# Performance work log

Measured on AMD Instinct MI355X. Metric: run time of the kernel, lower is better.

The kernel has to match this reference:

```python
import jax, jax.numpy as jnp
import numpy as np
from jax import lax

B, S, E, DF, H, L, V, T = 32, 512, 512, 2048, 8, 2, 30000, 12
START, STOP = 10, 11
NEG = -10000.0


def setup_inputs() -> dict:
    key = jax.random.key(0)
    ks = jax.random.split(key, 12)
    g = lambda i, shape, sc=0.02: jax.random.normal(ks[i], shape, jnp.float32) * sc
    trans = jax.random.normal(ks[9], (T, T), jnp.float32)
    trans = trans.at[START, :].set(NEG).at[:, STOP].set(NEG)
    return {
        "sentence": jax.random.randint(ks[0], (B, S), 0, V),
        "seq_len": jax.random.randint(ks[1], (B,), 1, S + 1),
        "tags": jax.random.randint(ks[2], (B, S), 0, 10),
        "emb": g(3, (V, E), 1.0),
        "attn_in_w": g(4, (L, 3 * E, E)), "attn_in_b": jnp.zeros((L, 3 * E)),
        "attn_out_w": g(5, (L, E, E)), "attn_out_b": jnp.zeros((L, E)),
        "ln1_g": jnp.ones((L, E)), "ln1_b": jnp.zeros((L, E)),
        "ln2_g": jnp.ones((L, E)), "ln2_b": jnp.zeros((L, E)),
        "ff1_w": g(6, (L, DF, E)), "ff1_b": jnp.zeros((L, DF)),
        "ff2_w": g(7, (L, E, DF)), "ff2_b": jnp.zeros((L, E)),
        "tag_w": g(8, (T, E)), "tag_b": jnp.zeros((T,)),
        "transitions": trans,
    }


def _ln(x, g, b):
    m = x.mean(-1, keepdims=True)
    v = ((x - m) ** 2).mean(-1, keepdims=True)
    return (x - m) / jnp.sqrt(v + 1e-5) * g + b


def _mha(x, w_in, b_in, w_out, b_out):
    b_, s_, e_ = x.shape
    d = e_ // H
    qkv = x @ w_in.T + b_in
    q, k, v = jnp.split(qkv, 3, axis=-1)
    split = lambda t: t.reshape(b_, s_, H, d).transpose(0, 2, 1, 3)
    q, k, v = split(q), split(k), split(v)
    att = jax.nn.softmax(jnp.einsum('bhqd,bhkd->bhqk', q, k) / np.sqrt(d).astype(np.float32), axis=-1)
    o = jnp.einsum('bhqk,bhkd->bhqd', att, v).transpose(0, 2, 1, 3).reshape(b_, s_, e_)
    return o @ w_out.T + b_out


def _forward_impl(sentence, seq_len, tags, emb, attn_in_w, attn_in_b, attn_out_w,
                  attn_out_b, ln1_g, ln1_b, ln2_g, ln2_b, ff1_w, ff1_b, ff2_w,
                  ff2_b, tag_w, tag_b, transitions):
    # Transformer encoder features (dropout in eval mode -> identity)
    x = emb[sentence]  # (B,S,E)
    for l in range(L):
        x = _ln(x + _mha(x, attn_in_w[l], attn_in_b[l], attn_out_w[l], attn_out_b[l]), ln1_g[l], ln1_b[l])
        h = jax.nn.relu(x @ ff1_w[l].T + ff1_b[l]) @ ff2_w[l].T + ff2_b[l]
        x = _ln(x + h, ln2_g[l], ln2_b[l])
    feats = x @ tag_w.T + tag_b  # (B,S,T)

    # CRF forward algorithm (log-semiring scan, masked by seq_len)
    alpha0 = jnp.full((B, T), NEG, feats.dtype).at[:, START].set(0.0)

    def step(alpha, xs):
        emit_t, t = xs  # emit_t: (B,T)
        new = emit_t + jax.nn.logsumexp(alpha[:, None, :] + transitions[None, :, :], axis=-1)
        return jnp.where((t < seq_len)[:, None], new, alpha), None

    alpha, _ = lax.scan(step, alpha0, (feats.transpose(1, 0, 2), jnp.arange(S)))
    fwd_score = jax.nn.logsumexp(alpha + transitions[STOP][None, :], axis=-1)  # (B,)

    # gold score (vectorized _score_sentence)
    tags_ext = jnp.concatenate([jnp.full((B, 1), START, tags.dtype), tags], axis=1)  # (B,S+1)
    mask = jnp.arange(S)[None, :] < seq_len[:, None]  # (B,S)
    trans_sc = jnp.where(mask, transitions[tags_ext[:, 1:], tags_ext[:, :-1]], 0.0).sum(-1)
    emit_sc = jnp.where(mask, jnp.take_along_axis(feats, tags[:, :, None], axis=2)[..., 0], 0.0).sum(-1)
    last_tag = jnp.take_along_axis(tags_ext, seq_len[:, None], axis=1)[:, 0]
    gold = trans_sc + emit_sc + transitions[STOP, last_tag]

    return jnp.mean(fwd_score - gold)


def reference(sentence, seq_len, tags, emb, attn_in_w, attn_in_b, attn_out_w,
              attn_out_b, ln1_g, ln1_b, ln2_g, ln2_b, ff1_w, ff1_b, ff2_w,
              ff2_b, tag_w, tag_b, transitions):
    return _forward_impl(sentence, seq_len, tags, emb, attn_in_w, attn_in_b,
                         attn_out_w, attn_out_b, ln1_g, ln1_b, ln2_g, ln2_b,
                         ff1_w, ff1_b, ff2_w, ff2_b, tag_w, tag_b, transitions)
```

## Files before the change

### kernel.cpp

```cpp
#include <hip/hip_runtime.h>
#include <hip/hip_bf16.h>

#define BB 32
#define SSZ 512
#define EE 512
#define DFF 2048
#define HH 8
#define LL 2
#define TT 12
#define START_TAG 10
#define STOP_TAG 11
#define CB 8
#define CM (CB * SSZ)
#define NCHUNK (BB / CB)
#define NBH (CB * HH)
#define NBH_ALL (BB * HH)
#define NCHK 8

typedef __hip_bfloat16 bf16;
typedef __attribute__((ext_vector_type(8))) short short8;
typedef __attribute__((ext_vector_type(4))) float f32x4;

__device__ __forceinline__ float b2f(bf16 x) { return __bfloat162float(x); }
__device__ __forceinline__ float ldw(const void* p, size_t i, bool isbf) {
  return isbf ? __bfloat162float(((const bf16*)p)[i]) : ((const float*)p)[i];
}

__device__ __forceinline__ void gl_lds16(const bf16* g, bf16* l) {
  __builtin_amdgcn_global_load_lds(
      (const __attribute__((address_space(1))) void*)g,
      (__attribute__((address_space(3))) void*)l, 16, 0, 0);
}

__device__ __forceinline__ void stg128(const bf16* __restrict__ G, int ldk,
                                       int row0, int col0, bf16* lds0,
                                       int w, int l) {
#pragma unroll
  for (int q = 0; q < 2; ++q) {
    int lr = q * 64 + w * 8 + (l >> 3);
    int gs = (l & 7) ^ (lr & 7);
    gl_lds16(G + (size_t)(row0 + lr) * ldk + col0 + gs * 8,
             lds0 + (q * 64 + w * 8) * 64);
  }
}

__device__ __forceinline__ short8 ldfrag(const bf16* T, int row, int gr) {
  return *(const short8*)&T[row * 64 + ((gr ^ (row & 7)) << 3)];
}

__global__ void k_detect(const void* trans, int* dflag) {
  if (threadIdx.x == 0) {
    const unsigned short* u = (const unsigned short*)trans;
    dflag[0] = (u[START_TAG * TT] == 0xC61C && u[START_TAG * TT + 1] == 0xC61C) ? 1 : 0;
  }
}

__global__ void k_cvt(const void* src, bf16* dst, long n, const int* dflag) {
  bool isbf = dflag[0] != 0;
  for (long i = (long)blockIdx.x * 256 + threadIdx.x; i < n; i += (long)gridDim.x * 256)
    dst[i] = __float2bfloat16(ldw(src, i, isbf));
}

__global__ void k_embed(const int* sent, const void* emb, bf16* xb, const int* dflag) {
  bool isbf = dflag[0] != 0;
  int tok = blockIdx.x;
  int v = sent[tok];
  bf16* xo = xb + (size_t)tok * EE;
  for (int i = threadIdx.x; i < EE; i += 256)
    xo[i] = __float2bfloat16(ldw(emb, (size_t)v * EE + i, isbf));
}

template <int BN>
__global__ __launch_bounds__(512, 2) void k_mgemm256(
    const bf16* __restrict__ A, const bf16* __restrict__ W,
    const void* __restrict__ bias, size_t boff, bf16* __restrict__ Cb,
    bf16* __restrict__ vtout, int M, int N, int K, int relu,
    const int* __restrict__ dflag) {
  constexpr int WN = BN / 64;
  constexpr int WM = 8 / WN;
  constexpr int RPW = 256 / WM;
  constexpr int MFR = RPW / 16;
  constexpr int QW = MFR / 4;
  constexpr int BH = BN / 128;
  constexpr int BUFSZ = 16384 + BN * 64;
  extern __shared__ __align__(16) bf16 Sh[];
  const bool isbf = dflag[0] != 0;
  const int tid = threadIdx.x;
  const int l = tid & 63;
  const int w = tid >> 6;
  const int wm = w / WN, wn = w % WN;
  const int lrow = l & 15, lk = l >> 4;
  const int m0 = blockIdx.x * 256, n0 = blockIdx.y * BN;

  f32x4 acc[MFR][4];
#pragma unroll
  for (int i = 0; i < MFR; ++i)
#pragma unroll
    for (int j = 0; j < 4; ++j) acc[i][j] = (f32x4){0.f, 0.f, 0.f, 0.f};

  const int NIT = K >> 7;

#pragma unroll
  for (int p = 0; p < 2; ++p) {
    bf16* Ab = Sh + p * BUFSZ;
    bf16* Bb = Ab + 16384;
    stg128(A, K, m0, p * 64, Ab, w, l);
    stg128(A, K, m0 + 128, p * 64, Ab + 8192, w, l);
#pragma unroll
    for (int h = 0; h < BH; ++h)
      stg128(W, K, n0 + h * 128, p * 64, Bb + h * 8192, w, l);
  }
  if (BN == 256) asm volatile("s_waitcnt vmcnt(8)" ::: "memory");
  else asm volatile("s_waitcnt vmcnt(6)" ::: "memory");
  __builtin_amdgcn_sched_barrier(0);
  __builtin_amdgcn_s_barrier();

#define LDAQ(q)                                                               \
  do {                                                                        \
    _Pragma("unroll") for (int mi = 0; mi < QW; ++mi)                         \
        _Pragma("unroll") for (int kb = 0; kb < 2; ++kb)                      \
            aq[q][mi][kb] = ldfrag(                                           \
                Ab, wm * RPW + ((q)*QW + mi) * 16 + lrow, kb * 4 + lk);       \
  } while (0)

#define MMQ(q)                                                                \
  do {                                                                        \
    __builtin_amdgcn_s_setprio(1);                                            \
    _Pragma("unroll") for (int mi = 0; mi < QW; ++mi)                         \
        _Pragma("unroll") for (int kb = 0; kb < 2; ++kb)                      \
            _Pragma("unroll") for (int nf = 0; nf < 4; ++nf)                  \
                acc[(q)*QW + mi][nf] =                                        \
                    __builtin_amdgcn_mfma_f32_16x16x32_bf16(                  \
                        aq[q][mi][kb], bfr[kb][nf], acc[(q)*QW + mi][nf],     \
                        0, 0, 0);                                             \
    __builtin_amdgcn_s_setprio(0);                                            \
  } while (0)

#pragma unroll 1
  for (int i = 0; i < NIT; ++i) {
    const bool more = (i + 1 < NIT);
#pragma unroll
    for (int hh = 0; hh < 2; ++hh) {
      bf16* Ab = Sh + hh * BUFSZ;
      bf16* Bb = Ab + 16384;
      const int kc2 = (2 * i + 2 + hh) << 6;
      short8 bfr[2][4];
      short8 aq[4][QW][2];
#pragma unroll
      for (int kb = 0; kb < 2; ++kb)
#pragma unroll
        for (int nf = 0; nf < 4; ++nf)
          bfr[kb][nf] = ldfrag(Bb, wn * 64 + nf * 16 + lrow, kb * 4 + lk);
      LDAQ(0);
      MMQ(0);
      __builtin_amdgcn_s_barrier();
      LDAQ(1);
      LDAQ(2);
      MMQ(1);
      __builtin_amdgcn_s_barrier();
      LDAQ(3);
      if (more) {
#pragma unroll
        for (int h = 0; h < BH; ++h)
          stg128(W, K, n0 + h * 128, kc2, Bb + h * 8192, w, l);
      }
      MMQ(2);
      asm volatile("s_waitcnt lgkmcnt(0)" ::: "memory");
      __builtin_amdgcn_sched_barrier(0);
      __builtin_amdgcn_s_barrier();
      if (more) {
        stg128(A, K, m0, kc2, Ab, w, l);
        stg128(A, K, m0 + 128, kc2, Ab + 8192, w, l);
      }
      MMQ(3);
      if (more) {
        if (BN == 256) asm volatile("s_waitcnt vmcnt(8)" ::: "memory");
        else asm volatile("s_waitcnt vmcnt(6)" ::: "memory");
      } else {
        asm volatile("s_waitcnt vmcnt(0)" ::: "memory");
      }
      __builtin_amdgcn_sched_barrier(0);
      __builtin_amdgcn_s_barrier();
    }
  }
#undef LDAQ
#undef MMQ

  const bool vpath = (BN == 256) && (vtout != nullptr) && (n0 >= 1024);
  if (!vpath) {
#pragma unroll
    for (int nf = 0; nf < 4; ++nf) {
      const int c = wn * 64 + nf * 16 + lrow;
      const float bia = ldw(bias, boff + n0 + c, isbf);
#pragma unroll
      for (int mf = 0; mf < MFR; ++mf)
#pragma unroll
        for (int r = 0; r < 4; ++r) {
          const int row = wm * RPW + mf * 16 + lk * 4 + r;
          float v = acc[mf][nf][r] + bia;
          if (relu) v = fmaxf(v, 0.f);
          Sh[row * BN + (c ^ (((row >> 2) & 7) << 4))] = __float2bfloat16(v);
        }
    }
    __syncthreads();
    constexpr int GPR = BN / 8;
    constexpr int RPP = 512 / GPR;
#pragma unroll
    for (int p = 0; p < 256 / RPP; ++p) {
      const int row = p * RPP + tid / GPR;
      const int g = tid % GPR;
      *(uint4*)(Cb + (size_t)(m0 + row) * N + n0 + g * 8) =
          *(const uint4*)&Sh[row * BN + ((g * 8) ^ (((row >> 2) & 7) << 4))];
    }
  } else {
    const int pos0 = m0 & 511;
    const int blb = (m0 >> 9) * 8;
#pragma unroll
    for (int nf = 0; nf < 4; ++nf) {
      const int c = wn * 64 + nf * 16 + lrow;
      const float bia = ldw(bias, boff + n0 + c, isbf);
#pragma unroll
      for (int mf = 0; mf < MFR; ++mf)
#pragma unroll
        for (int r = 0; r < 4; ++r) {
          const int row = wm * RPW + mf * 16 + lk * 4 + r;
          Sh[c * 256 + (row ^ (((c >> 2) & 7) << 4))] =
              __float2bfloat16(acc[mf][nf][r] + bia);
        }
    }
    __syncthreads();
#pragma unroll
    for (int p = 0; p < 16; ++p) {
      const int cc = p * 16 + (tid >> 5);
      const int g = tid & 31;
      const int vc = n0 - 1024 + cc;
      *(uint4*)(vtout + ((size_t)(blb + (vc >> 6)) * 64 + (vc & 63)) * 512 +
                pos0 + g * 8) =
          *(const uint4*)&Sh[cc * 256 + ((g * 8) ^ (((cc >> 2) & 7) << 4))];
    }
  }
}

#define LDK 68
#define LDP 72
__global__ __launch_bounds__(256) void k_flash(const bf16* __restrict__ qkv,
                                               const bf16* __restrict__ vt,
                                               bf16* __restrict__ ctx) {
  const int bh = blockIdx.x;
  const int bl = bh >> 3, h = bh & 7;
  const int m0 = blockIdx.y * 128;
  const int tid = threadIdx.x;
  const int lane = tid & 63;
  const int w = tid >> 6;
  const int lrow = lane & 15, lk = lane >> 4;

  __shared__ bf16 Ks[64 * LDK];
  __shared__ bf16 Vs[64 * LDK];
  __shared__ bf16 Ps[4][32 * LDP];

  short8 qf[2][2];
  {
    const bf16* Qb = qkv + (size_t)(bl * SSZ + m0 + w * 32) * 1536 + h * 64;
#pragma unroll
    for (int mf = 0; mf < 2; ++mf)
#pragma unroll
      for (int kb = 0; kb < 2; ++kb)
        qf[mf][kb] = *(const short8*)(Qb + (size_t)(mf * 16 + lrow) * 1536 + kb * 32 + lk * 8);
  }

  f32x4 acc_o[2][4];
  float lsum[2][4];
#pragma unroll
  for (int mf = 0; mf < 2; ++mf) {
#pragma unroll
    for (int nf = 0; nf < 4; ++nf) acc_o[mf][nf] = (f32x4){0.f, 0.f, 0.f, 0.f};
#pragma unroll
    for (int r = 0; r < 4; ++r) lsum[mf][r] = 0.f;
  }

  for (int kt = 0; kt < 8; ++kt) {
#pragma unroll
    for (int i = 0; i < 2; ++i) {
      int cc = tid + i * 256;
      int row = cc >> 3, seg = cc & 7;
      *(uint4*)&Ks[row * LDK + seg * 8] = *(const uint4*)(
          qkv + (size_t)(bl * SSZ + kt * 64 + row) * 1536 + 512 + h * 64 + seg * 8);
      *(uint4*)&Vs[row * LDK + seg * 8] = *(const uint4*)(
          vt + ((size_t)bh * 64 + row) * SSZ + kt * 64 + seg * 8);
    }
    __syncthreads();
    f32x4 s[2][4];
#pragma unroll
    for (int mf = 0; mf < 2; ++mf)
#pragma unroll
      for (int nf = 0; nf < 4; ++nf) s[mf][nf] = (f32x4){0.f, 0.f, 0.f, 0.f};
#pragma unroll
    for (int kb = 0; kb < 2; ++kb) {
      short8 bk[4];
#pragma unroll
      for (int nf = 0; nf < 4; ++nf)
        bk[nf] = *(const short8*)&Ks[(nf * 16 + lrow) * LDK + kb * 32 + lk * 8];
#pragma unroll
      for (int mf = 0; mf < 2; ++mf)
#pragma unroll
        for (int nf = 0; nf < 4; ++nf)
          s[mf][nf] = __builtin_amdgcn_mfma_f32_16x16x32_bf16(qf[mf][kb], bk[nf],
                                                              s[mf][nf], 0, 0, 0);
    }
#pragma unroll
    for (int mf = 0; mf < 2; ++mf)
#pragma unroll
      for (int r = 0; r < 4; ++r) {
        float p0 = __expf(0.125f * s[mf][0][r]);
        float p1 = __expf(0.125f * s[mf][1][r]);
        float p2 = __expf(0.125f * s[mf][2][r]);
        float p3 = __expf(0.125f * s[mf][3][r]);
        s[mf][0][r] = p0; s[mf][1][r] = p1; s[mf][2][r] = p2; s[mf][3][r] = p3;
        lsum[mf][r] += (p0 + p1) + (p2 + p3);
      }
#pragma unroll
    for (int mf = 0; mf < 2; ++mf)
#pragma unroll
      for (int nf = 0; nf < 4; ++nf)
#pragma unroll
        for (int r = 0; r < 4; ++r)
          Ps[w][(mf * 16 + lk * 4 + r) * LDP + nf * 16 + lrow] =
              __float2bfloat16(s[mf][nf][r]);
#pragma unroll
    for (int kb = 0; kb < 2; ++kb) {
      short8 ap[2], bv[4];
#pragma unroll
      for (int mf = 0; mf < 2; ++mf)
        ap[mf] = *(const short8*)&Ps[w][(mf * 16 + lrow) * LDP + kb * 32 + lk * 8];
#pragma unroll
      for (int nf = 0; nf < 4; ++nf)
        bv[nf] = *(const short8*)&Vs[(nf * 16 + lrow) * LDK + kb * 32 + lk * 8];
#pragma unroll
      for (int mf = 0; mf < 2; ++mf)
#pragma unroll
        for (int nf = 0; nf < 4; ++nf)
          acc_o[mf][nf] = __builtin_amdgcn_mfma_f32_16x16x32_bf16(ap[mf], bv[nf],
                                                                  acc_o[mf][nf], 0, 0, 0);
    }
    __syncthreads();
  }
#pragma unroll
  for (int mf = 0; mf < 2; ++mf) {
#pragma unroll
    for (int r = 0; r < 4; ++r) {
      float ls = lsum[mf][r];
      ls += __shfl_xor(ls, 1, 64);
      ls += __shfl_xor(ls, 2, 64);
      ls += __shfl_xor(ls, 4, 64);
      ls += __shfl_xor(ls, 8, 64);
      float inv = 1.f / ls;
      int q = m0 + w * 32 + mf * 16 + lk * 4 + r;
#pragma unroll
      for (int nf = 0; nf < 4; ++nf)
        ctx[((size_t)(bl * SSZ + q)) * EE + h * 64 + nf * 16 + lrow] =
            __float2bfloat16(acc_o[mf][nf][r] * inv);
    }
  }
}

__global__ void k_ln_res(bf16* xb, const bf16* hb, const void* g,
                         const void* be, size_t goff, const int* dflag) {
  bool isbf = dflag[0] != 0;
  int tok = blockIdx.x, tid = threadIdx.x;
  size_t base = (size_t)tok * EE;
  float v0 = b2f(xb[base + tid]) + b2f(hb[base + tid]);
  float v1 = b2f(xb[base + tid + 256]) + b2f(hb[base + tid + 256]);
  float s = v0 + v1, ss = v0 * v0 + v1 * v1;
#pragma unroll
  for (int off = 32; off > 0; off >>= 1) {
    s += __shfl_down(s, off, 64);
    ss += __shfl_down(ss, off, 64);
  }
  __shared__ float ps[4], pss[4];
  __shared__ float mean_s, rstd_s;
  int w = tid >> 6;
  if ((tid & 63) == 0) { ps[w] = s; pss[w] = ss; }
  __syncthreads();
  if (tid == 0) {
    float S_ = ps[0] + ps[1] + ps[2] + ps[3];
    float SS_ = pss[0] + pss[1] + pss[2] + pss[3];
    float mu = S_ / (float)EE;
    float var = SS_ / (float)EE - mu * mu;
    mean_s = mu;
    rstd_s = rsqrtf(var + 1e-5f);
  }
  __syncthreads();
  float mu = mean_s, rs = rstd_s;
  float r0 = (v0 - mu) * rs * ldw(g, goff + tid, isbf) + ldw(be, goff + tid, isbf);
  float r1 = (v1 - mu) * rs * ldw(g, goff + tid + 256, isbf) + ldw(be, goff + tid + 256, isbf);
  xb[base + tid] = __float2bfloat16(r0);
  xb[base + tid + 256] = __float2bfloat16(r1);
}

__global__ void k_feats(const bf16* xb, const bf16* tgw, const void* tgb,
                        float* feats, const int* dflag) {
  bool isbf = dflag[0] != 0;
  int m = blockIdx.x * 4 + (threadIdx.x >> 6);
  int lane = threadIdx.x & 63;
  uint4 raw = *(const uint4*)(xb + (size_t)m * EE + lane * 8);
  const bf16* rb = (const bf16*)&raw;
  float xv[8];
#pragma unroll
  for (int j = 0; j < 8; ++j) xv[j] = b2f(rb[j]);
#pragma unroll
  for (int t = 0; t < TT; ++t) {
    uint4 wraw = *(const uint4*)(tgw + t * EE + lane * 8);
    const bf16* wb = (const bf16*)&wraw;
    float s = 0.f;
#pragma unroll
    for (int j = 0; j < 8; ++j) s += xv[j] * b2f(wb[j]);
#pragma unroll
    for (int off = 32; off > 0; off >>= 1) s += __shfl_down(s, off, 64);
    if (lane == 0) feats[(size_t)m * TT + t] = s + ldw(tgb, t, isbf);
  }
}

__global__ void k_crf1(const float* feats, const int* seq_len, const void* trans_in,
                       float* cmat, const int* dflag) {
  bool isbf = dflag[0] != 0;
  int c = blockIdx.x, b = blockIdx.y;
  int tid = threadIdx.x;
  __shared__ float tr[144];
  __shared__ float abuf[2][144];
  if (tid < 144) tr[tid] = ldw(trans_in, tid, isbf);
  bool act = tid < 144;
  int i = tid / 12, j = tid % 12;
  if (act) abuf[0][tid] = (i == j) ? 0.f : -1e30f;
  __syncthreads();
  float trrow[12];
  if (act) {
#pragma unroll
    for (int k = 0; k < 12; ++k) trrow[k] = tr[i * 12 + k];
  }
  int len = seq_len[b];
  int t0 = c * 64;
  int t1 = min(len, t0 + 64);
  int cur = 0;
  for (int t = t0; t < t1; ++t) {
    float nv = 0.f;
    if (act) {
      float m = -1e30f, v[12];
#pragma unroll
      for (int k = 0; k < 12; ++k) {
        v[k] = trrow[k] + abuf[cur][k * 12 + j];
        m = fmaxf(m, v[k]);
      }
      float s = 0.f;
#pragma unroll
      for (int k = 0; k < 12; ++k) s += __expf(v[k] - m);
      nv = feats[((size_t)b * SSZ + t) * TT + i] + m + __logf(s);
    }
    if (act) abuf[cur ^ 1][tid] = nv;
    __syncthreads();
    cur ^= 1;
  }
  if (act) cmat[((size_t)b * NCHK + c) * 144 + tid] = abuf[cur][tid];
}

__global__ void k_crf2(const float* cmat, const float* feats, const int* tags,
                       const int* seq_len, const void* trans_in, float* bscore,
                       const int* dflag) {
  bool isbf = dflag[0] != 0;
  int b = blockIdx.x;
  int tid = threadIdx.x;
  __shared__ float tr[144];
  __shared__ float tbuf[2][144];
  __shared__ float alpha_sh[12];
  if (tid < 144) tr[tid] = ldw(trans_in, tid, isbf);
  bool act = tid < 144;
  int i = tid / 12, j = tid % 12;
  if (act) tbuf[0][tid] = cmat[((size_t)b * NCHK) * 144 + tid];
  __syncthreads();
  int cur = 0;
  for (int c = 1; c < NCHK; ++c) {
    float nv = 0.f;
    if (act) {
      const float* Cc = cmat + ((size_t)b * NCHK + c) * 144;
      float m = -1e30f, v[12];
#pragma unroll
      for (int k = 0; k < 12; ++k) {
        v[k] = Cc[i * 12 + k] + tbuf[cur][k * 12 + j];
        m = fmaxf(m, v[k]);
      }
      float s = 0.f;
#pragma unroll
      for (int k = 0; k < 12; ++k) s += __expf(v[k] - m);
      nv = m + __logf(s);
    }
    if (act) tbuf[cur ^ 1][tid] = nv;
    __syncthreads();
    cur ^= 1;
  }
  if (tid < 12) {
    float m = -1e30f, v[12];
#pragma unroll
    for (int k = 0; k < 12; ++k) {
      float a0 = (k == START_TAG) ? 0.f : -10000.f;
      v[k] = tbuf[cur][tid * 12 + k] + a0;
      m = fmaxf(m, v[k]);
    }
    float s = 0.f;
#pragma unroll
    for (int k = 0; k < 12; ++k) s += __expf(v[k] - m);
    alpha_sh[tid] = m + __logf(s);
  }
  __syncthreads();
  if (tid < 64) {
    int lane = tid;
    int len = seq_len[b];
    float part = 0.f;
    for (int s = lane; s < len; s += 64) {
      int ct = tags[b * SSZ + s];
      int pv = (s == 0) ? START_TAG : tags[b * SSZ + s - 1];
      part += tr[ct * 12 + pv] + feats[((size_t)b * SSZ + s) * TT + ct];
    }
#pragma unroll
    for (int off = 32; off > 0; off >>= 1) part += __shfl_down(part, off, 64);
    if (lane == 0) {
      float m = -1e30f;
#pragma unroll
      for (int k = 0; k < 12; ++k) m = fmaxf(m, alpha_sh[k] + tr[STOP_TAG * 12 + k]);
      float s = 0.f;
#pragma unroll
      for (int k = 0; k < 12; ++k) s += __expf(alpha_sh[k] + tr[STOP_TAG * 12 + k] - m);
      float fwd = m + __logf(s);
      int last = tags[b * SSZ + len - 1];
      bscore[b] = fwd - (part + tr[STOP_TAG * 12 + last]);
    }
  }
}

__global__ void k_final(const float* bscore, float* out) {
  int tid = threadIdx.x;
  float v = (tid < BB) ? bscore[tid] : 0.f;
#pragma unroll
  for (int off = 32; off > 0; off >>= 1) v += __shfl_down(v, off, 64);
  if (tid == 0) out[0] = v / (float)BB;
}

extern "C" void kernel_launch(void* const* d_in, const int* in_sizes, int n_in,
                              void* d_out, int out_size, void* d_ws, size_t ws_size,
                              hipStream_t stream) {
  const int* sentence = (const int*)d_in[0];
  const int* seq_len = (const int*)d_in[1];
  const int* tags = (const int*)d_in[2];
  const void* emb = d_in[3];
  const void* attn_in_w = d_in[4];
  const void* attn_in_b = d_in[5];
  const void* attn_out_w = d_in[6];
  const void* attn_out_b = d_in[7];
  const void* ln1_g = d_in[8];
  const void* ln1_b = d_in[9];
  const void* ln2_g = d_in[10];
  const void* ln2_b = d_in[11];
  const void* ff1_w = d_in[12];
  const void* ff1_b = d_in[13];
  const void* ff2_w = d_in[14];
  const void* ff2_b = d_in[15];
  const void* tag_w = d_in[16];
  const void* tag_b = d_in[17];
  const void* transitions = d_in[18];

  static int attr_done = 0;
  if (!attr_done) {
    (void)hipFuncSetAttribute((const void*)&k_mgemm256<256>,
                              hipFuncAttributeMaxDynamicSharedMemorySize, 131072);
    (void)hipFuncSetAttribute((const void*)&k_mgemm256<128>,
                              hipFuncAttributeMaxDynamicSharedMemorySize, 131072);
    attr_done = 1;
  }

  const int M = BB * SSZ;
  const size_t WEL = (size_t)LL * 3 * EE * EE + (size_t)LL * EE * EE +
                     (size_t)LL * DFF * EE + (size_t)LL * EE * DFF + (size_t)TT * EE;

  size_t o = 0;
  size_t f_feats = o; o += (size_t)M * TT;
  size_t f_bsc = o; o += 64;
  size_t f_cmat = o; o += (size_t)BB * NCHK * 144;
  size_t f_dflag = o; o += 16;
  size_t f_xb = o; o += (size_t)M * EE / 2;
  size_t f_hb = o; o += (size_t)M * EE / 2;
  size_t f_ctxb = o; o += (size_t)M * EE / 2;
  size_t f_act = o; o += (size_t)M * DFF / 2;
  size_t f_vt = o; o += (size_t)NBH_ALL * 64 * SSZ / 2;
  size_t f_w = o; o += (WEL + 1) / 2 + 8;
  size_t need_full = o * 4;
  bool full = ws_size >= need_full;

  float* ws = (float*)d_ws;
  if (full) {
    float* feats = ws + f_feats;
    float* bsc = ws + f_bsc;
    float* cmat = ws + f_cmat;
    int* dflag = (int*)(ws + f_dflag);
    bf16* xb = (bf16*)(ws + f_xb);
    bf16* hb = (bf16*)(ws + f_hb);
    bf16* ctxb = (bf16*)(ws + f_ctxb);
    bf16* act = (bf16*)(ws + f_act);
    bf16* vt = (bf16*)(ws + f_vt);
    bf16* w_aiw = (bf16*)(ws + f_w);
    bf16* w_aow = w_aiw + (size_t)LL * 3 * EE * EE;
    bf16* w_f1 = w_aow + (size_t)LL * EE * EE;
    bf16* w_f2 = w_f1 + (size_t)LL * DFF * EE;
    bf16* w_tg = w_f2 + (size_t)LL * EE * DFF;

    k_detect<<<dim3(1), dim3(64), 0, stream>>>(transitions, dflag);
    k_cvt<<<dim3(1024), dim3(256), 0, stream>>>(attn_in_w, w_aiw, (long)LL * 3 * EE * EE, dflag);
    k_cvt<<<dim3(512), dim3(256), 0, stream>>>(attn_out_w, w_aow, (long)LL * EE * EE, dflag);
    k_cvt<<<dim3(1024), dim3(256), 0, stream>>>(ff1_w, w_f1, (long)LL * DFF * EE, dflag);
    k_cvt<<<dim3(1024), dim3(256), 0, stream>>>(ff2_w, w_f2, (long)LL * EE * DFF, dflag);
    k_cvt<<<dim3(24), dim3(256), 0, stream>>>(tag_w, w_tg, (long)TT * EE, dflag);
    k_embed<<<dim3(M), dim3(256), 0, stream>>>(sentence, emb, xb, dflag);

    for (int l = 0; l < LL; ++l) {
      k_mgemm256<256><<<dim3(M / 256, 6), dim3(512), 131072, stream>>>(
          xb, w_aiw + (size_t)l * 3 * EE * EE, attn_in_b, (size_t)l * 3 * EE,
          act, vt, M, 3 * EE, EE, 0, dflag);
      k_flash<<<dim3(NBH_ALL, SSZ / 128), dim3(256), 0, stream>>>(act, vt, ctxb);
      k_mgemm256<128><<<dim3(M / 256, EE / 128), dim3(512), 98304, stream>>>(
          ctxb, w_aow + (size_t)l * EE * EE, attn_out_b, (size_t)l * EE,
          hb, (bf16*)nullptr, M, EE, EE, 0, dflag);
      k_ln_res<<<dim3(M), dim3(256), 0, stream>>>(xb, hb, ln1_g, ln1_b,
                                                  (size_t)l * EE, dflag);
      k_mgemm256<256><<<dim3(M / 256, DFF / 256), dim3(512), 131072, stream>>>(
          xb, w_f1 + (size_t)l * DFF * EE, ff1_b, (size_t)l * DFF,
          act, (bf16*)nullptr, M, DFF, EE, 1, dflag);
      k_mgemm256<128><<<dim3(M / 256, EE / 128), dim3(512), 98304, stream>>>(
          act, w_f2 + (size_t)l * EE * DFF, ff2_b, (size_t)l * EE,
          hb, (bf16*)nullptr, M, EE, DFF, 0, dflag);
      k_ln_res<<<dim3(M), dim3(256), 0, stream>>>(xb, hb, ln2_g, ln2_b,
                                                  (size_t)l * EE, dflag);
    }
    k_feats<<<dim3(M / 4), dim3(256), 0, stream>>>(xb, w_tg, tag_b, feats, dflag);
    k_crf1<<<dim3(NCHK, BB), dim3(192), 0, stream>>>(feats, seq_len, transitions, cmat, dflag);
    k_crf2<<<dim3(BB), dim3(192), 0, stream>>>(cmat, feats, tags, seq_len, transitions, bsc, dflag);
    k_final<<<dim3(1), dim3(64), 0, stream>>>(bsc, (float*)d_out);
  } else {
    float* feats = ws;
    float* bsc = feats + (size_t)M * TT;
    float* cmat = bsc + 64;
    int* dflag = (int*)(cmat + (size_t)BB * NCHK * 144 + 16);
    bf16* xb = (bf16*)(dflag + 16);
    bf16* hb = xb + (size_t)M * EE;
    bf16* qkvb = hb + (size_t)CM * EE;
    bf16* ctxb = qkvb + (size_t)CM * 1536;
    bf16* ffh = ctxb + (size_t)CM * EE;
    bf16* vt = ffh + (size_t)CM * DFF;
    bf16* w_aiw = vt + (size_t)NBH * 64 * SSZ;
    bf16* w_aow = w_aiw + (size_t)LL * 3 * EE * EE;
    bf16* w_f1 = w_aow + (size_t)LL * EE * EE;
    bf16* w_f2 = w_f1 + (size_t)LL * DFF * EE;
    bf16* w_tg = w_f2 + (size_t)LL * EE * DFF;

    k_detect<<<dim3(1), dim3(64), 0, stream>>>(transitions, dflag);
    k_cvt<<<dim3(1024), dim3(256), 0, stream>>>(attn_in_w, w_aiw, (long)LL * 3 * EE * EE, dflag);
    k_cvt<<<dim3(512), dim3(256), 0, stream>>>(attn_out_w, w_aow, (long)LL * EE * EE, dflag);
    k_cvt<<<dim3(1024), dim3(256), 0, stream>>>(ff1_w, w_f1, (long)LL * DFF * EE, dflag);
    k_cvt<<<dim3(1024), dim3(256), 0, stream>>>(ff2_w, w_f2, (long)LL * EE * DFF, dflag);
    k_cvt<<<dim3(24), dim3(256), 0, stream>>>(tag_w, w_tg, (long)TT * EE, dflag);
    k_embed<<<dim3(M), dim3(256), 0, stream>>>(sentence, emb, xb, dflag);

    for (int l = 0; l < LL; ++l) {
      for (int c = 0; c < NCHUNK; ++c) {
        bf16* xbc = xb + (size_t)c * CM * EE;
        k_mgemm256<256><<<dim3(CM / 256, 6), dim3(512), 131072, stream>>>(
            xbc, w_aiw + (size_t)l * 3 * EE * EE, attn_in_b, (size_t)l * 3 * EE,
            qkvb, vt, CM, 3 * EE, EE, 0, dflag);
        k_flash<<<dim3(NBH, SSZ / 128), dim3(256), 0, stream>>>(qkvb, vt, ctxb);
        k_mgemm256<128><<<dim3(CM / 256, EE / 128), dim3(512), 98304, stream>>>(
            ctxb, w_aow + (size_t)l * EE * EE, attn_out_b, (size_t)l * EE,
            hb, (bf16*)nullptr, CM, EE, EE, 0, dflag);
        k_ln_res<<<dim3(CM), dim3(256), 0, stream>>>(xbc, hb, ln1_g, ln1_b,
                                                     (size_t)l * EE, dflag);
        k_mgemm256<256><<<dim3(CM / 256, DFF / 256), dim3(512), 131072, stream>>>(
            xbc, w_f1 + (size_t)l * DFF * EE, ff1_b, (size_t)l * DFF,
            ffh, (bf16*)nullptr, CM, DFF, EE, 1, dflag);
        k_mgemm256<128><<<dim3(CM / 256, EE / 128), dim3(512), 98304, stream>>>(
            ffh, w_f2 + (size_t)l * EE * DFF, ff2_b, (size_t)l * EE,
            hb, (bf16*)nullptr, CM, EE, DFF, 0, dflag);
        k_ln_res<<<dim3(CM), dim3(256), 0, stream>>>(xbc, hb, ln2_g, ln2_b,
                                                     (size_t)l * EE, dflag);
      }
    }
    k_feats<<<dim3(M / 4), dim3(256), 0, stream>>>(xb, w_tg, tag_b, feats, dflag);
    k_crf1<<<dim3(NCHK, BB), dim3(192), 0, stream>>>(feats, seq_len, transitions, cmat, dflag);
    k_crf2<<<dim3(BB), dim3(192), 0, stream>>>(cmat, feats, tags, seq_len, transitions, bsc, dflag);
    k_final<<<dim3(1), dim3(64), 0, stream>>>(bsc, (float*)d_out);
  }
}
```

Before: 696.9 us.

## Double-buffer K/V in flash attention with direct global-to-LDS loads and larger blocks

Measured after the change: 656.2 us, median of 2. 1.06x faster.

```diff
diff --git a/kernel.cpp b/kernel.cpp
--- a/kernel.cpp
+++ b/kernel.cpp
@@ -241,22 +241,20 @@
   }
 }
 
-#define LDK 68
 #define LDP 72
-__global__ __launch_bounds__(256) void k_flash(const bf16* __restrict__ qkv,
+__global__ __launch_bounds__(512) void k_flash(const bf16* __restrict__ qkv,
                                                const bf16* __restrict__ vt,
                                                bf16* __restrict__ ctx) {
+  extern __shared__ __align__(16) bf16 Fs[];
   const int bh = blockIdx.x;
   const int bl = bh >> 3, h = bh & 7;
-  const int m0 = blockIdx.y * 128;
+  const int m0 = blockIdx.y * 256;
   const int tid = threadIdx.x;
-  const int lane = tid & 63;
+  const int l = tid & 63;
   const int w = tid >> 6;
-  const int lrow = lane & 15, lk = lane >> 4;
-
-  __shared__ bf16 Ks[64 * LDK];
-  __shared__ bf16 Vs[64 * LDK];
-  __shared__ bf16 Ps[4][32 * LDP];
+  const int lrow = l & 15, lk = l >> 4;
+
+  bf16* Psw = Fs + 16384 + w * (32 * LDP);
 
   short8 qf[2][2];
   {
@@ -278,17 +276,25 @@
     for (int r = 0; r < 4; ++r) lsum[mf][r] = 0.f;
   }
 
+  const int srow = w * 8 + (l >> 3);
+  const int gsw = (l & 7) ^ (srow & 7);
+  const bf16* Ksrc = qkv + (size_t)(bl * SSZ + srow) * 1536 + 512 + h * 64 + gsw * 8;
+  const bf16* Vsrc = vt + ((size_t)bh * 64 + srow) * SSZ + gsw * 8;
+#define STAGE_KV(kt, b)                                                       \
+  do {                                                                        \
+    gl_lds16(Ksrc + (size_t)(kt)*64 * 1536, Fs + (b)*8192 + w * 512);         \
+    gl_lds16(Vsrc + (kt)*64, Fs + (b)*8192 + 4096 + w * 512);                 \
+  } while (0)
+
+  STAGE_KV(0, 0);
+  __syncthreads();
+
   for (int kt = 0; kt < 8; ++kt) {
-#pragma unroll
-    for (int i = 0; i < 2; ++i) {
-      int cc = tid + i * 256;
-      int row = cc >> 3, seg = cc & 7;
-      *(uint4*)&Ks[row * LDK + seg * 8] = *(const uint4*)(
-          qkv + (size_t)(bl * SSZ + kt * 64 + row) * 1536 + 512 + h * 64 + seg * 8);
-      *(uint4*)&Vs[row * LDK + seg * 8] = *(const uint4*)(
-          vt + ((size_t)bh * 64 + row) * SSZ + kt * 64 + seg * 8);
-    }
-    __syncthreads();
+    const int cur = kt & 1;
+    if (kt < 7) STAGE_KV(kt + 1, cur ^ 1);
+    const bf16* Ks = Fs + cur * 8192;
+    const bf16* Vs = Ks + 4096;
+
     f32x4 s[2][4];
 #pragma unroll
     for (int mf = 0; mf < 2; ++mf)
@@ -299,7 +305,7 @@
       short8 bk[4];
 #pragma unroll
       for (int nf = 0; nf < 4; ++nf)
-        bk[nf] = *(const short8*)&Ks[(nf * 16 + lrow) * LDK + kb * 32 + lk * 8];
+        bk[nf] = ldfrag(Ks, nf * 16 + lrow, kb * 4 + lk);
 #pragma unroll
       for (int mf = 0; mf < 2; ++mf)
 #pragma unroll
@@ -324,17 +330,17 @@
       for (int nf = 0; nf < 4; ++nf)
 #pragma unroll
         for (int r = 0; r < 4; ++r)
-          Ps[w][(mf * 16 + lk * 4 + r) * LDP + nf * 16 + lrow] =
+          Psw[(mf * 16 + lk * 4 + r) * LDP + nf * 16 + lrow] =
               __float2bfloat16(s[mf][nf][r]);
 #pragma unroll
     for (int kb = 0; kb < 2; ++kb) {
       short8 ap[2], bv[4];
 #pragma unroll
       for (int mf = 0; mf < 2; ++mf)
-        ap[mf] = *(const short8*)&Ps[w][(mf * 16 + lrow) * LDP + kb * 32 + lk * 8];
+        ap[mf] = *(const short8*)&Psw[(mf * 16 + lrow) * LDP + kb * 32 + lk * 8];
 #pragma unroll
       for (int nf = 0; nf < 4; ++nf)
-        bv[nf] = *(const short8*)&Vs[(nf * 16 + lrow) * LDK + kb * 32 + lk * 8];
+        bv[nf] = ldfrag(Vs, nf * 16 + lrow, kb * 4 + lk);
 #pragma unroll
       for (int mf = 0; mf < 2; ++mf)
 #pragma unroll
@@ -344,6 +350,7 @@
     }
     __syncthreads();
   }
+#undef STAGE_KV
 #pragma unroll
   for (int mf = 0; mf < 2; ++mf) {
 #pragma unroll
@@ -572,8 +579,11 @@
                               hipFuncAttributeMaxDynamicSharedMemorySize, 131072);
     (void)hipFuncSetAttribute((const void*)&k_mgemm256<128>,
                               hipFuncAttributeMaxDynamicSharedMemorySize, 131072);
+    (void)hipFuncSetAttribute((const void*)&k_flash,
+                              hipFuncAttributeMaxDynamicSharedMemorySize, 131072);
     attr_done = 1;
   }
+  const int FLDS = (16384 + 8 * 32 * LDP) * 2;
 
   const int M = BB * SSZ;
   const size_t WEL = (size_t)LL * 3 * EE * EE + (size_t)LL * EE * EE +
@@ -622,7 +632,7 @@
       k_mgemm256<256><<<dim3(M / 256, 6), dim3(512), 131072, stream>>>(
           xb, w_aiw + (size_t)l * 3 * EE * EE, attn_in_b, (size_t)l * 3 * EE,
           act, vt, M, 3 * EE, EE, 0, dflag);
-      k_flash<<<dim3(NBH_ALL, SSZ / 128), dim3(256), 0, stream>>>(act, vt, ctxb);
+      k_flash<<<dim3(NBH_ALL, 2), dim3(512), FLDS, stream>>>(act, vt, ctxb);
       k_mgemm256<128><<<dim3(M / 256, EE / 128), dim3(512), 98304, stream>>>(
           ctxb, w_aow + (size_t)l * EE * EE, attn_out_b, (size_t)l * EE,
           hb, (bf16*)nullptr, M, EE, EE, 0, dflag);
@@ -672,7 +682,7 @@
         k_mgemm256<256><<<dim3(CM / 256, 6), dim3(512), 131072, stream>>>(
             xbc, w_aiw + (size_t)l * 3 * EE * EE, attn_in_b, (size_t)l * 3 * EE,
             qkvb, vt, CM, 3 * EE, EE, 0, dflag);
-        k_flash<<<dim3(NBH, SSZ / 128), dim3(256), 0, stream>>>(qkvb, vt, ctxb);
+        k_flash<<<dim3(NBH, 2), dim3(512), FLDS, stream>>>(qkvb, vt, ctxb);
         k_mgemm256<128><<<dim3(CM / 256, EE / 128), dim3(512), 98304, stream>>>(
             ctxb, w_aow + (size_t)l * EE * EE, attn_out_b, (size_t)l * EE,
             hb, (bf16*)nullptr, CM, EE, EE, 0, dflag);
```
